# Kernel tuning notes

Measured on AMD Instinct MI355X. Metric: run time of the kernel, lower is better.

Reference implementation:

```python
import jax, jax.numpy as jnp
import numpy as np

B, L, C = 16, 4096, 32
D = 512
W = 24                  # rolling window
LAGS = [3, 5, 7]
MAXLEN = 5000
EPS = 1e-5


def setup_inputs() -> dict:
    key = jax.random.key(0)
    ks = jax.random.split(key, 8)
    return {
        "x": jax.random.normal(ks[0], (B, L, C), jnp.float32),
        "conv_w": jax.random.normal(ks[1], (D, C * (5 + len(LAGS)), 3), jnp.float32) * 0.05,
        "conv_b": jnp.zeros((D,), jnp.float32),
        "learned_pe": jax.random.normal(ks[2], (1, MAXLEN, D), jnp.float32) * (1.0 / np.sqrt(D)),
        "tape_pos": jax.random.normal(ks[3], (MAXLEN, D), jnp.float32) * 0.02,
        "tproj_w": jax.random.normal(ks[4], (D, D), jnp.float32) * 0.02,
        "tproj_b": jnp.zeros((D,), jnp.float32),
        "mixer_w": jax.random.normal(ks[5], (D, 2 * D), jnp.float32) * 0.02,
        "mixer_b": jnp.zeros((D,), jnp.float32),
        "g_c": jnp.ones((D,), jnp.float32), "b_c": jnp.zeros((D,), jnp.float32),
        "g_f": jnp.ones((D,), jnp.float32), "b_f": jnp.zeros((D,), jnp.float32),
        "g_l": jnp.ones((D,), jnp.float32), "b_l": jnp.zeros((D,), jnp.float32),
        "g_t": jnp.ones((D,), jnp.float32), "b_t": jnp.zeros((D,), jnp.float32),
        "weight_params": jnp.array([0.25, 0.25, 0.25, 0.25], jnp.float32),
    }


def _layer_norm(h, g, b):
    m = jnp.mean(h, axis=-1, keepdims=True)
    v = jnp.mean((h - m) ** 2, axis=-1, keepdims=True)
    return g * (h - m) / jnp.sqrt(v + EPS) + b


def reference(x, conv_w, conv_b, learned_pe, tape_pos, tproj_w, tproj_b,
              mixer_w, mixer_b, g_c, b_c, g_f, b_f, g_l, b_l, g_t, b_t,
              weight_params):
    Bx, Lx, Cx = x.shape
    # --- RollingFeatureExtractor: replicate-pad left, sliding mean/max/min/std
    xp = jnp.pad(x, ((0, 0), (W - 1, 0), (0, 0)), mode="edge")          # [B, L+W-1, C]
    win = jnp.stack([xp[:, i:i + Lx, :] for i in range(W)], axis=2)       # [B, L, W, C]
    w_mean = jnp.mean(win, axis=2)
    w_max = jnp.max(win, axis=2)
    w_min = jnp.min(win, axis=2)
    w_var = jnp.sum((win - w_mean[:, :, None, :]) ** 2, axis=2) / (W - 1)  # unbiased, torch.std default
    w_std = jnp.sqrt(w_var)
    x_stats = jnp.concatenate([x, w_mean, w_max, w_min, w_std], axis=-1)  # [B, L, 5C]
    # --- lag differences (replicate pad left by max lag)
    ml = max(LAGS)
    xl = jnp.pad(x, ((0, 0), (ml, 0), (0, 0)), mode="edge")
    x_lags = jnp.concatenate([x - xl[:, ml - l:ml - l + Lx, :] for l in LAGS], axis=-1)  # [B, L, 3C]
    comb = jnp.concatenate([x_stats, x_lags], axis=-1)                    # [B, L, 8C]
    # --- TokenEmbedding: Conv1d k=3, circular padding
    h = comb.transpose(0, 2, 1)                                           # [B, 8C, L]
    h = jnp.pad(h, ((0, 0), (0, 0), (1, 1)), mode="wrap")
    h = jax.lax.conv_general_dilated(h, conv_w, (1,), "VALID",
                                     dimension_numbers=("NCH", "OIH", "NCH"))
    h = h + conv_b[None, :, None]
    combined_emb = _layer_norm(h.transpose(0, 2, 1), g_c, b_c)            # [B, L, D]
    # --- fixed sinusoidal PE (constant / detached)
    pos = jnp.arange(Lx)
    div = jnp.exp(jnp.arange(0, D, 2).astype(x.dtype) * (-(np.log(10000.0) / D)))
    ang = pos[:, None].astype(x.dtype) * div[None, :]                     # [L, D/2]
    pe_fixed_tab = jnp.zeros((Lx, D), x.dtype).at[:, 0::2].set(jnp.sin(ang)).at[:, 1::2].set(jnp.cos(ang))
    pe_fixed = _layer_norm(pe_fixed_tab, g_f, b_f)[None]                  # [1, L, D]
    # --- learnable PE
    pe_learned = _layer_norm(learned_pe[:, :Lx], g_l, b_l)                # [1, L, D]
    # --- tAPE: token proj + learned pos embedding -> mixer linear
    pe = tape_pos[pos]                                                    # [L, D]
    tok = combined_emb @ tproj_w.T + tproj_b                              # [B, L, D]
    mixed = jnp.concatenate([tok, jnp.broadcast_to(pe[None], tok.shape)], axis=-1)
    pe_tape = _layer_norm(mixed @ mixer_w.T + mixer_b, g_t, b_t)          # [B, L, D]
    # --- softmax-weighted sum (dropout is identity in eval)
    w = jax.nn.softmax(weight_params)
    return (w[0] * combined_emb + w[1] * pe_fixed + w[2] * pe_learned + w[3] * pe_tape)
```

## Files before the change

kernel.cpp:

```cpp
#include <hip/hip_runtime.h>
#include <stdint.h>


typedef unsigned short u16;
using short8  = __attribute__((ext_vector_type(8))) short;
using floatx4 = __attribute__((ext_vector_type(4))) float;
typedef __attribute__((address_space(1))) const unsigned int u32_as1;
typedef __attribute__((address_space(3))) unsigned int       u32_as3;

static __device__ __forceinline__ u16 f2b(float f) {
  unsigned u = __float_as_uint(f);
  u += 0x7FFFu + ((u >> 16) & 1u);
  return (u16)(u >> 16);
}
static __device__ __forceinline__ float b2f(u16 h) {
  return __uint_as_float(((unsigned)h) << 16);
}

__global__ __launch_bounds__(256) void prep_all(
    const float* __restrict__ x,
    const float* __restrict__ conv_w, const float* __restrict__ mixer_w,
    const float* __restrict__ tproj_w, const float* __restrict__ tape_pos,
    const float* __restrict__ tproj_b, const float* __restrict__ mixer_b,
    const float* __restrict__ learned_pe,
    const float* __restrict__ gf, const float* __restrict__ bf_,
    const float* __restrict__ gl, const float* __restrict__ bl,
    u16* __restrict__ W1, u16* __restrict__ A_m1, u16* __restrict__ M2t,
    u16* __restrict__ tprojT, u16* __restrict__ tape_bf,
    float* __restrict__ bias2, u16* __restrict__ pf_tab,
    u16* __restrict__ pl_tab, u16* __restrict__ comb) {
  __shared__ float sx[87 * 32];
  const int bx = blockIdx.x;
  if (bx < 12800) {
    int i = bx * 256 + threadIdx.x;
    if (i < 393216) {
      int d = i / 768, rem = i - d * 768;
      int j = rem >> 8, c = rem & 255;
      W1[i] = f2b(conv_w[(d * 256 + c) * 3 + j]);
    } else if (i < 393216 + 262144) {
      int k = i - 393216; int p = k >> 9, r = k & 511;
      A_m1[k] = f2b(mixer_w[p * 1024 + r]);
    } else if (i < 393216 + 524288) {
      int k = i - 393216 - 262144; int p = k >> 9, r = k & 511;
      M2t[k] = f2b(mixer_w[p * 1024 + 512 + r]);
    } else if (i < 393216 + 786432) {
      int k = i - 393216 - 524288; int q = k >> 9, r = k & 511;
      tprojT[k] = f2b(tproj_w[r * 512 + q]);
    } else if (i < 393216 + 786432 + 2097152) {
      int k = i - 393216 - 786432;
      tape_bf[k] = f2b(tape_pos[k]);
    }
    return;
  }
  if (bx < 12802) {
    int p = (bx - 12800) * 256 + threadIdx.x;
    if (p < 512) {
      float s = mixer_b[p];
      for (int r = 0; r < 512; ++r) s += mixer_w[p * 1024 + r] * tproj_b[r];
      bias2[p] = s;
    }
    return;
  }
  if (bx < 13826) {
    int row = (bx - 12802) * 4 + (threadIdx.x >> 6);
    int lane = threadIdx.x & 63;
    size_t base = (size_t)row * 512 + lane * 8;
    float v[8]; float s1 = 0.f, s2 = 0.f;
    #pragma unroll
    for (int e = 0; e < 8; ++e) {
      int d = lane * 8 + e;
      int de = d & ~1;
      float div = expf((float)de * (-9.210340371976184f / 512.f));
      float ang = (float)row * div;
      v[e] = (d & 1) ? cosf(ang) : sinf(ang);
      s1 += v[e]; s2 += v[e] * v[e];
    }
    #pragma unroll
    for (int off = 32; off; off >>= 1) { s1 += __shfl_xor(s1, off); s2 += __shfl_xor(s2, off); }
    float mean = s1 * (1.f / 512.f);
    float inv = rsqrtf(fmaxf(s2 * (1.f / 512.f) - mean * mean, 0.f) + 1e-5f);
    short8 o;
    #pragma unroll
    for (int e = 0; e < 8; ++e) {
      int d = lane * 8 + e;
      o[e] = (short)f2b(gf[d] * ((v[e] - mean) * inv) + bf_[d]);
    }
    *(short8*)(pf_tab + base) = o;
    const float4* lp = (const float4*)(learned_pe + base);
    float4 a = lp[0], bq = lp[1];
    float u[8] = {a.x, a.y, a.z, a.w, bq.x, bq.y, bq.z, bq.w};
    s1 = 0.f; s2 = 0.f;
    #pragma unroll
    for (int e = 0; e < 8; ++e) { s1 += u[e]; s2 += u[e] * u[e]; }
    #pragma unroll
    for (int off = 32; off; off >>= 1) { s1 += __shfl_xor(s1, off); s2 += __shfl_xor(s2, off); }
    mean = s1 * (1.f / 512.f);
    inv = rsqrtf(fmaxf(s2 * (1.f / 512.f) - mean * mean, 0.f) + 1e-5f);
    #pragma unroll
    for (int e = 0; e < 8; ++e) {
      int d = lane * 8 + e;
      o[e] = (short)f2b(gl[d] * ((u[e] - mean) * inv) + bl[d]);
    }
    *(short8*)(pl_tab + base) = o;
    return;
  }
  const int fb = bx - 13826;
  const int b = fb >> 6, l0 = (fb & 63) * 64;
  for (int idx = threadIdx.x; idx < 87 * 32; idx += 256) {
    int r = idx >> 5, c = idx & 31;
    int ls = l0 - 23 + r; if (ls < 0) ls = 0;
    sx[idx] = x[((size_t)b * 4096 + ls) * 32 + c];
  }
  __syncthreads();
  const int c = threadIdx.x & 31, lr0 = threadIdx.x >> 5;
  for (int pass = 0; pass < 8; ++pass) {
    int lr = pass * 8 + lr0;
    int l = l0 + lr;
    float w[24];
    float s = 0.f, mx = -3.4e38f, mn = 3.4e38f;
    #pragma unroll
    for (int i = 0; i < 24; ++i) {
      float v = sx[(lr + i) * 32 + c];
      w[i] = v; s += v; mx = fmaxf(mx, v); mn = fminf(mn, v);
    }
    float mean = s * (1.f / 24.f);
    float ssd = 0.f;
    #pragma unroll
    for (int i = 0; i < 24; ++i) { float d = w[i] - mean; ssd += d * d; }
    float sd = sqrtf(fmaxf(ssd, 0.f) * (1.f / 23.f));
    float xv = w[23];
    float lag3 = xv - sx[(lr + 20) * 32 + c];
    float lag5 = xv - sx[(lr + 18) * 32 + c];
    float lag7 = xv - sx[(lr + 16) * 32 + c];
    size_t base = ((size_t)b * 4096 + l) * 256 + c;
    comb[base +   0] = f2b(xv);
    comb[base +  32] = f2b(mean);
    comb[base +  64] = f2b(mx);
    comb[base +  96] = f2b(mn);
    comb[base + 128] = f2b(sd);
    comb[base + 160] = f2b(lag3);
    comb[base + 192] = f2b(lag5);
    comb[base + 224] = f2b(lag7);
  }
}

static __device__ __forceinline__ void gemm_bt_dev(
    const u16* __restrict__ A, const u16* __restrict__ Bt,
    u16* __restrict__ outp, int K, int ldc,
    const float* __restrict__ bias, int m0, int n0,
    u16* lA, u16* lB) {
  const int tid = threadIdx.x;
  const int wave = tid >> 6, lane = tid & 63;
  const int wm = (wave & 1) * 64, wn = (wave >> 1) * 64;
  const int quad = lane >> 4, r16 = lane & 15;
  const int rowT = tid >> 3, col8 = tid & 7;

  floatx4 acc[4][4];
  #pragma unroll
  for (int i = 0; i < 4; ++i)
    #pragma unroll
    for (int j = 0; j < 4; ++j) acc[i][j] = (floatx4){0.f, 0.f, 0.f, 0.f};

  for (int kk = 0; kk < K; kk += 64) {
    __syncthreads();
    #pragma unroll
    for (int it = 0; it < 4; ++it) {
      int rr = it * 32 + rowT;
      const u16* ga = A  + (size_t)(m0 + rr) * K + kk + col8 * 8;
      const u16* gb = Bt + (size_t)(n0 + rr) * K + kk + col8 * 8;
      __builtin_amdgcn_global_load_lds((u32_as1*)ga, (u32_as3*)&lA[rr * 64 + col8 * 8], 16, 0, 0);
      __builtin_amdgcn_global_load_lds((u32_as1*)gb, (u32_as3*)&lB[rr * 64 + col8 * 8], 16, 0, 0);
    }
    __syncthreads();
    #pragma unroll
    for (int ks = 0; ks < 64; ks += 32) {
      short8 af[4], bfr[4];
      #pragma unroll
      for (int i = 0; i < 4; ++i)
        af[i] = *(const short8*)&lA[(wm + i * 16 + r16) * 64 + ks + quad * 8];
      #pragma unroll
      for (int j = 0; j < 4; ++j)
        bfr[j] = *(const short8*)&lB[(wn + j * 16 + r16) * 64 + ks + quad * 8];
      #pragma unroll
      for (int i = 0; i < 4; ++i)
        #pragma unroll
        for (int j = 0; j < 4; ++j)
          acc[i][j] = __builtin_amdgcn_mfma_f32_16x16x32_bf16(af[i], bfr[j], acc[i][j], 0, 0, 0);
    }
  }
  #pragma unroll
  for (int i = 0; i < 4; ++i) {
    #pragma unroll
    for (int rr = 0; rr < 4; ++rr) {
      int m = m0 + wm + i * 16 + quad * 4 + rr;
      #pragma unroll
      for (int j = 0; j < 4; ++j) {
        int n = n0 + wn + j * 16 + r16;
        float v = acc[i][j][rr];
        if (bias) v += bias[n];
        outp[(size_t)m * ldc + n] = f2b(v);
      }
    }
  }
}

__global__ __launch_bounds__(256) void gemm_bt_both(
    const u16* __restrict__ A_m1, const u16* __restrict__ tprojT,
    u16* __restrict__ Wf, const u16* __restrict__ tape_bf,
    const u16* __restrict__ M2t, u16* __restrict__ ctab_bf,
    const float* __restrict__ bias2) {
  __shared__ __align__(16) u16 lA[128 * 64];
  __shared__ __align__(16) u16 lB[128 * 64];
  const int bx = blockIdx.x;
  if (bx < 16) {
    gemm_bt_dev(A_m1, tprojT, Wf, 512, 512, nullptr,
                (bx & 3) * 128, (bx >> 2) * 128, lA, lB);
  } else {
    const int i = bx - 16;
    gemm_bt_dev(tape_bf, M2t, ctab_bf, 512, 512, bias2,
                (i & 31) * 128, (i >> 5) * 128, lA, lB);
  }
}


#define STAGE_A(SRCEXPR)                                                       \
  _Pragma("unroll")                                                            \
  for (int it = 0; it < 2; ++it) {                                             \
    int id = it * 256 + tid, row = id >> 3, c = id & 7;                        \
    int cg = ((c ^ (row & 7)) << 3);                                           \
    const u16* gsrc = (SRCEXPR);                                               \
    __builtin_amdgcn_global_load_lds((u32_as1*)gsrc,                           \
        (u32_as3*)(smem + id * 16), 16, 0, 0);                                 \
  }
#define STAGE_B(SRCEXPR)                                                       \
  _Pragma("unroll")                                                            \
  for (int it = 0; it < 16; ++it) {                                            \
    int id = it * 256 + tid, row = id >> 3, c = id & 7;                        \
    int cg = ((c ^ (row & 7)) << 3);                                           \
    const u16* gsrc = (SRCEXPR);                                               \
    __builtin_amdgcn_global_load_lds((u32_as1*)gsrc,                           \
        (u32_as3*)(smem + 8192 + id * 16), 16, 0, 0);                          \
  }

__global__ __launch_bounds__(256, 2) void gemm_conv_pre(
    const u16* __restrict__ comb, const u16* __restrict__ W1,
    const float* __restrict__ conv_b, const float* __restrict__ g_c,
    const float* __restrict__ b_c, const u16* __restrict__ Wf,
    const u16* __restrict__ ctab_bf, const u16* __restrict__ pf_tab,
    const u16* __restrict__ pl_tab, const float* __restrict__ g_t,
    const float* __restrict__ b_t, const float* __restrict__ wp,
    u16* __restrict__ ce, float* __restrict__ out) {
  __shared__ __align__(16) char smem[73728];
  __shared__ __align__(16) float sGB[1024];
  float* sG = sGB;
  float* sB = sGB + 512;
  u16* lA = (u16*)smem;
  u16* lB = (u16*)(smem + 8192);
  u16* lT = (u16*)smem;

  const int tid = threadIdx.x;
  if (tid < 128) {
    ((float4*)sG)[tid] = ((const float4*)g_c)[tid];
    ((float4*)sB)[tid] = ((const float4*)b_c)[tid];
  }
  const int m0 = blockIdx.x * 64;
  const int b = m0 >> 12, l0 = m0 & 4095;
  const int w = tid >> 6, lane = tid & 63;
  const int quad = lane >> 4, r16 = lane & 15;
  const int wn = w * 128;

  floatx4 acc[4][8];
  #pragma unroll
  for (int i = 0; i < 4; ++i)
    #pragma unroll
    for (int jj = 0; jj < 8; ++jj) acc[i][jj] = (floatx4){0.f, 0.f, 0.f, 0.f};

  for (int kk = 0; kk < 768; kk += 64) {
    const int jsh = kk >> 8, kc = kk & 255;
    __syncthreads();
    STAGE_A(comb + (((size_t)b * 4096 + ((l0 + row + jsh - 1 + 4096) & 4095)) << 8) + kc + cg)
    STAGE_B(W1 + (size_t)row * 768 + kk + cg)
    __syncthreads();
    #pragma unroll
    for (int ks = 0; ks < 64; ks += 32) {
      short8 af[4];
      #pragma unroll
      for (int i = 0; i < 4; ++i) {
        int row = i * 16 + r16;
        af[i] = *(const short8*)&lA[row * 64 + ((((ks >> 3) + quad) ^ (row & 7)) << 3)];
      }
      #pragma unroll
      for (int jj = 0; jj < 8; ++jj) {
        int row = wn + jj * 16 + r16;
        short8 bf = *(const short8*)&lB[row * 64 + ((((ks >> 3) + quad) ^ (row & 7)) << 3)];
        #pragma unroll
        for (int i = 0; i < 4; ++i)
          acc[i][jj] = __builtin_amdgcn_mfma_f32_16x16x32_bf16(bf, af[i], acc[i][jj], 0, 0, 0);
      }
    }
  }
  __syncthreads();
  #pragma unroll
  for (int jj = 0; jj < 8; ++jj) {
    int n = wn + jj * 16 + quad * 4;
    float4 b4 = *(const float4*)&conv_b[n];
    #pragma unroll
    for (int i = 0; i < 4; ++i) {
      ushort4 pk;
      pk.x = f2b(acc[i][jj][0] + b4.x);
      pk.y = f2b(acc[i][jj][1] + b4.y);
      pk.z = f2b(acc[i][jj][2] + b4.z);
      pk.w = f2b(acc[i][jj][3] + b4.w);
      *(ushort4*)(lT + (size_t)(i * 16 + r16) * 520 + n) = pk;
    }
  }
  __syncthreads();
  {
    const int orow = tid >> 2, part = tid & 3;
    u16* rowp = lT + (size_t)orow * 520;
    float s1 = 0.f, s2 = 0.f;
    #pragma unroll
    for (int k = 0; k < 16; ++k) {
      short8 t8 = *(const short8*)(rowp + (part + k * 4) * 8);
      #pragma unroll
      for (int e = 0; e < 8; ++e) {
        float f = b2f((u16)t8[e]); s1 += f; s2 += f * f;
      }
    }
    s1 += __shfl_xor(s1, 1); s2 += __shfl_xor(s2, 1);
    s1 += __shfl_xor(s1, 2); s2 += __shfl_xor(s2, 2);
    float mean = s1 * (1.f / 512.f);
    float inv = rsqrtf(fmaxf(s2 * (1.f / 512.f) - mean * mean, 0.f) + 1e-5f);
    size_t mrow = (size_t)(m0 + orow) * 512;
    #pragma unroll
    for (int k = 0; k < 16; ++k) {
      int c8 = part + k * 4;
      short8 t8 = *(const short8*)(rowp + c8 * 8);
      short8 o;
      #pragma unroll
      for (int e = 0; e < 8; ++e) {
        int d = c8 * 8 + e;
        o[e] = (short)f2b(sG[d] * ((b2f((u16)t8[e]) - mean) * inv) + sB[d]);
      }
      *(short8*)(ce + mrow + c8 * 8) = o;
    }
  }
  __syncthreads();
  if (tid < 128) {
    ((float4*)sG)[tid] = ((const float4*)g_t)[tid];
    ((float4*)sB)[tid] = ((const float4*)b_t)[tid];
  }

  floatx4 acc2[4][8];
  #pragma unroll
  for (int i = 0; i < 4; ++i)
    #pragma unroll
    for (int jj = 0; jj < 8; ++jj) acc2[i][jj] = (floatx4){0.f, 0.f, 0.f, 0.f};

  for (int kk = 0; kk < 512; kk += 64) {
    __syncthreads();
    STAGE_A(ce + (size_t)(m0 + row) * 512 + kk + cg)
    STAGE_B(Wf + (size_t)row * 512 + kk + cg)
    __syncthreads();
    #pragma unroll
    for (int ks = 0; ks < 64; ks += 32) {
      short8 af[4];
      #pragma unroll
      for (int i = 0; i < 4; ++i) {
        int row = i * 16 + r16;
        af[i] = *(const short8*)&lA[row * 64 + ((((ks >> 3) + quad) ^ (row & 7)) << 3)];
      }
      #pragma unroll
      for (int jj = 0; jj < 8; ++jj) {
        int row = wn + jj * 16 + r16;
        short8 bf = *(const short8*)&lB[row * 64 + ((((ks >> 3) + quad) ^ (row & 7)) << 3)];
        #pragma unroll
        for (int i = 0; i < 4; ++i)
          acc2[i][jj] = __builtin_amdgcn_mfma_f32_16x16x32_bf16(bf, af[i], acc2[i][jj], 0, 0, 0);
      }
    }
  }
  __syncthreads();
  #pragma unroll
  for (int jj = 0; jj < 8; ++jj) {
    int n = wn + jj * 16 + quad * 4;
    #pragma unroll
    for (int i = 0; i < 4; ++i) {
      ushort4 pk;
      pk.x = f2b(acc2[i][jj][0]);
      pk.y = f2b(acc2[i][jj][1]);
      pk.z = f2b(acc2[i][jj][2]);
      pk.w = f2b(acc2[i][jj][3]);
      *(ushort4*)(lT + (size_t)(i * 16 + r16) * 520 + n) = pk;
    }
  }
  __syncthreads();
  const int orow = tid >> 2, part = tid & 3;
  const int m = m0 + orow, l = l0 + orow;
  const u16* rowp = lT + (size_t)orow * 520;
  const size_t lrow = (size_t)l * 512, mrow = (size_t)m * 512;
  float s1 = 0.f, s2 = 0.f;
  #pragma unroll
  for (int k = 0; k < 16; ++k) {
    int c8 = part + k * 4;
    short8 t8 = *(const short8*)(rowp + c8 * 8);
    short8 ct = *(const short8*)(ctab_bf + lrow + c8 * 8);
    #pragma unroll
    for (int e = 0; e < 8; ++e) {
      float f = b2f((u16)t8[e]) + b2f((u16)ct[e]);
      s1 += f; s2 += f * f;
    }
  }
  s1 += __shfl_xor(s1, 1); s2 += __shfl_xor(s2, 1);
  s1 += __shfl_xor(s1, 2); s2 += __shfl_xor(s2, 2);
  float mean = s1 * (1.f / 512.f);
  float inv = rsqrtf(fmaxf(s2 * (1.f / 512.f) - mean * mean, 0.f) + 1e-5f);

  float a0 = wp[0], a1 = wp[1], a2 = wp[2], a3 = wp[3];
  float mxw = fmaxf(fmaxf(a0, a1), fmaxf(a2, a3));
  float e0 = expf(a0 - mxw), e1 = expf(a1 - mxw), e2 = expf(a2 - mxw), e3 = expf(a3 - mxw);
  float invs = 1.f / (e0 + e1 + e2 + e3);
  float w0 = e0 * invs, w1 = e1 * invs, w2 = e2 * invs, w3 = e3 * invs;

  #pragma unroll
  for (int k = 0; k < 16; ++k) {
    int c8 = part + k * 4;
    short8 t8  = *(const short8*)(rowp + c8 * 8);
    short8 ct  = *(const short8*)(ctab_bf + lrow + c8 * 8);
    short8 c8v = *(const short8*)(ce + mrow + c8 * 8);
    short8 pf  = *(const short8*)(pf_tab + lrow + c8 * 8);
    short8 pl  = *(const short8*)(pl_tab + lrow + c8 * 8);
    float o[8];
    #pragma unroll
    for (int e = 0; e < 8; ++e) {
      int d = c8 * 8 + e;
      float f = b2f((u16)t8[e]) + b2f((u16)ct[e]);
      float pt = sG[d] * ((f - mean) * inv) + sB[d];
      o[e] = w0 * b2f((u16)c8v[e]) + w1 * b2f((u16)pf[e]) + w2 * b2f((u16)pl[e]) + w3 * pt;
    }
    float4* op = (float4*)(out + mrow + c8 * 8);
    op[0] = make_float4(o[0], o[1], o[2], o[3]);
    op[1] = make_float4(o[4], o[5], o[6], o[7]);
  }
}

extern "C" void kernel_launch(void* const* d_in, const int* in_sizes, int n_in,
                              void* d_out, int out_size, void* d_ws, size_t ws_size,
                              hipStream_t stream) {
  const float* x          = (const float*)d_in[0];
  const float* conv_w     = (const float*)d_in[1];
  const float* conv_b     = (const float*)d_in[2];
  const float* learned_pe = (const float*)d_in[3];
  const float* tape_pos   = (const float*)d_in[4];
  const float* tproj_w    = (const float*)d_in[5];
  const float* tproj_b    = (const float*)d_in[6];
  const float* mixer_w    = (const float*)d_in[7];
  const float* mixer_b    = (const float*)d_in[8];
  const float* g_c        = (const float*)d_in[9];
  const float* b_c        = (const float*)d_in[10];
  const float* g_f        = (const float*)d_in[11];
  const float* b_f        = (const float*)d_in[12];
  const float* g_l        = (const float*)d_in[13];
  const float* b_l        = (const float*)d_in[14];
  const float* g_t        = (const float*)d_in[15];
  const float* b_t        = (const float*)d_in[16];
  const float* wp         = (const float*)d_in[17];

  char* ws = (char*)d_ws;
  u16*  comb    = (u16*)(ws + 0);
  u16*  ce      = (u16*)(ws + 33554432);
  char* S       = ws + 100663296;
  u16*  W1      = (u16*)(S + 0);
  u16*  A_m1    = (u16*)(S + 786432);
  u16*  M2t     = (u16*)(S + 1310720);
  u16*  tprojT  = (u16*)(S + 1835008);
  u16*  tape_bf = (u16*)(S + 2359296);
  u16*  Wf      = (u16*)(S + 6553600);
  u16*  ctab_bf = (u16*)(S + 7077888);
  float* bias2  = (float*)(S + 11272192);
  u16*  pf_tab  = (u16*)(S + 11274240);
  u16*  pl_tab  = (u16*)(S + 15468544);

  prep_all<<<14850, 256, 0, stream>>>(x, conv_w, mixer_w, tproj_w, tape_pos,
                                      tproj_b, mixer_b, learned_pe,
                                      g_f, b_f, g_l, b_l,
                                      W1, A_m1, M2t, tprojT, tape_bf,
                                      bias2, pf_tab, pl_tab, comb);
  gemm_bt_both<<<144, 256, 0, stream>>>(A_m1, tprojT, Wf, tape_bf, M2t,
                                        ctab_bf, bias2);
  gemm_conv_pre<<<1024, 256, 0, stream>>>(comb, W1, conv_b, g_c, b_c,
                                          Wf, ctab_bf, pf_tab, pl_tab,
                                          g_t, b_t, wp, ce, (float*)d_out);
}
```

Measured before the change: 356.0 us.

## Double-buffer A tiles and give each wave a private B strip in fused GEMMs

```diff
diff --git a/kernel.cpp b/kernel.cpp
--- a/kernel.cpp
+++ b/kernel.cpp
@@ -223,23 +223,23 @@
 }
 
 
-#define STAGE_A(SRCEXPR)                                                       \
+#define STAGE_A2(BUFOFF, SRCEXPR)                                              \
   _Pragma("unroll")                                                            \
   for (int it = 0; it < 2; ++it) {                                             \
     int id = it * 256 + tid, row = id >> 3, c = id & 7;                        \
     int cg = ((c ^ (row & 7)) << 3);                                           \
     const u16* gsrc = (SRCEXPR);                                               \
     __builtin_amdgcn_global_load_lds((u32_as1*)gsrc,                           \
-        (u32_as3*)(smem + id * 16), 16, 0, 0);                                 \
-  }
-#define STAGE_B(SRCEXPR)                                                       \
+        (u32_as3*)(smem + (BUFOFF) + id * 16), 16, 0, 0);                      \
+  }
+#define STRIP_B(BPTR, LDB, KK)                                                 \
   _Pragma("unroll")                                                            \
   for (int it = 0; it < 16; ++it) {                                            \
-    int id = it * 256 + tid, row = id >> 3, c = id & 7;                        \
-    int cg = ((c ^ (row & 7)) << 3);                                           \
-    const u16* gsrc = (SRCEXPR);                                               \
+    int rl = it * 8 + (lane >> 3);                                             \
+    int cgb = (((lane & 7) ^ (rl & 7)) << 3);                                  \
+    const u16* gsrc = (BPTR) + (size_t)(wn + rl) * (LDB) + (KK) + cgb;         \
     __builtin_amdgcn_global_load_lds((u32_as1*)gsrc,                           \
-        (u32_as3*)(smem + 8192 + id * 16), 16, 0, 0);                          \
+        (u32_as3*)(stripB + it * 1024 + (lane << 4)), 16, 0, 0);               \
   }
 
 __global__ __launch_bounds__(256, 2) void gemm_conv_pre(
@@ -250,24 +250,18 @@
     const u16* __restrict__ pl_tab, const float* __restrict__ g_t,
     const float* __restrict__ b_t, const float* __restrict__ wp,
     u16* __restrict__ ce, float* __restrict__ out) {
-  __shared__ __align__(16) char smem[73728];
-  __shared__ __align__(16) float sGB[1024];
-  float* sG = sGB;
-  float* sB = sGB + 512;
-  u16* lA = (u16*)smem;
-  u16* lB = (u16*)(smem + 8192);
-  u16* lT = (u16*)smem;
+  __shared__ __align__(16) char smem[81920];
+  u16*   lT = (u16*)smem;
+  float* sG = (float*)(smem + 67584);
+  float* sB = (float*)(smem + 69632);
 
   const int tid = threadIdx.x;
-  if (tid < 128) {
-    ((float4*)sG)[tid] = ((const float4*)g_c)[tid];
-    ((float4*)sB)[tid] = ((const float4*)b_c)[tid];
-  }
   const int m0 = blockIdx.x * 64;
   const int b = m0 >> 12, l0 = m0 & 4095;
   const int w = tid >> 6, lane = tid & 63;
   const int quad = lane >> 4, r16 = lane & 15;
   const int wn = w * 128;
+  char* stripB = smem + 16384 + w * 16384;
 
   floatx4 acc[4][8];
   #pragma unroll
@@ -275,28 +269,49 @@
     #pragma unroll
     for (int jj = 0; jj < 8; ++jj) acc[i][jj] = (floatx4){0.f, 0.f, 0.f, 0.f};
 
-  for (int kk = 0; kk < 768; kk += 64) {
-    const int jsh = kk >> 8, kc = kk & 255;
-    __syncthreads();
-    STAGE_A(comb + (((size_t)b * 4096 + ((l0 + row + jsh - 1 + 4096) & 4095)) << 8) + kc + cg)
-    STAGE_B(W1 + (size_t)row * 768 + kk + cg)
-    __syncthreads();
+  STAGE_A2(0, comb + (((size_t)b * 4096 + ((l0 + row - 1 + 4096) & 4095)) << 8) + cg)
+  STRIP_B(W1, 768, 0)
+
+  for (int t = 0; t < 12; ++t) {
+    const int kk = t * 64;
+    __builtin_amdgcn_sched_barrier(0);
+    __builtin_amdgcn_s_barrier();
+    __builtin_amdgcn_sched_barrier(0);
+    if (t + 1 < 12) {
+      const int kk2 = kk + 64;
+      const int jsh = kk2 >> 8, kc = kk2 & 255;
+      STAGE_A2(((t + 1) & 1) * 8192,
+          comb + (((size_t)b * 4096 + ((l0 + row + jsh - 1 + 4096) & 4095)) << 8) + kc + cg)
+      asm volatile("s_waitcnt vmcnt(2)" ::: "memory");
+    } else {
+      asm volatile("s_waitcnt vmcnt(0)" ::: "memory");
+    }
+    __builtin_amdgcn_sched_barrier(0);
+    __builtin_amdgcn_s_barrier();
+    __builtin_amdgcn_sched_barrier(0);
+    const u16* lAc = (const u16*)(smem + (t & 1) * 8192);
     #pragma unroll
     for (int ks = 0; ks < 64; ks += 32) {
       short8 af[4];
       #pragma unroll
       for (int i = 0; i < 4; ++i) {
         int row = i * 16 + r16;
-        af[i] = *(const short8*)&lA[row * 64 + ((((ks >> 3) + quad) ^ (row & 7)) << 3)];
-      }
+        af[i] = *(const short8*)&lAc[row * 64 + ((((ks >> 3) + quad) ^ (row & 7)) << 3)];
+      }
+      __builtin_amdgcn_s_setprio(1);
       #pragma unroll
       for (int jj = 0; jj < 8; ++jj) {
-        int row = wn + jj * 16 + r16;
-        short8 bf = *(const short8*)&lB[row * 64 + ((((ks >> 3) + quad) ^ (row & 7)) << 3)];
+        int rl = jj * 16 + r16;
+        short8 bf = *(const short8*)(stripB + rl * 128 + ((((ks >> 3) + quad) ^ (rl & 7)) << 4));
         #pragma unroll
         for (int i = 0; i < 4; ++i)
           acc[i][jj] = __builtin_amdgcn_mfma_f32_16x16x32_bf16(bf, af[i], acc[i][jj], 0, 0, 0);
       }
+      __builtin_amdgcn_s_setprio(0);
+    }
+    if (t + 1 < 12) {
+      const int kk2 = kk + 64;
+      STRIP_B(W1, 768, kk2)
     }
   }
   __syncthreads();
@@ -314,6 +329,10 @@
       *(ushort4*)(lT + (size_t)(i * 16 + r16) * 520 + n) = pk;
     }
   }
+  if (tid < 128) {
+    ((float4*)sG)[tid] = ((const float4*)g_c)[tid];
+    ((float4*)sB)[tid] = ((const float4*)b_c)[tid];
+  }
   __syncthreads();
   {
     const int orow = tid >> 2, part = tid & 3;
@@ -346,10 +365,6 @@
     }
   }
   __syncthreads();
-  if (tid < 128) {
-    ((float4*)sG)[tid] = ((const float4*)g_t)[tid];
-    ((float4*)sB)[tid] = ((const float4*)b_t)[tid];
-  }
 
   floatx4 acc2[4][8];
   #pragma unroll
@@ -357,27 +372,46 @@
     #pragma unroll
     for (int jj = 0; jj < 8; ++jj) acc2[i][jj] = (floatx4){0.f, 0.f, 0.f, 0.f};
 
-  for (int kk = 0; kk < 512; kk += 64) {
-    __syncthreads();
-    STAGE_A(ce + (size_t)(m0 + row) * 512 + kk + cg)
-    STAGE_B(Wf + (size_t)row * 512 + kk + cg)
-    __syncthreads();
+  STAGE_A2(0, ce + (size_t)(m0 + row) * 512 + cg)
+  STRIP_B(Wf, 512, 0)
+
+  for (int t = 0; t < 8; ++t) {
+    const int kk = t * 64;
+    __builtin_amdgcn_sched_barrier(0);
+    __builtin_amdgcn_s_barrier();
+    __builtin_amdgcn_sched_barrier(0);
+    if (t + 1 < 8) {
+      STAGE_A2(((t + 1) & 1) * 8192,
+          ce + (size_t)(m0 + row) * 512 + kk + 64 + cg)
+      asm volatile("s_waitcnt vmcnt(2)" ::: "memory");
+    } else {
+      asm volatile("s_waitcnt vmcnt(0)" ::: "memory");
+    }
+    __builtin_amdgcn_sched_barrier(0);
+    __builtin_amdgcn_s_barrier();
+    __builtin_amdgcn_sched_barrier(0);
+    const u16* lAc = (const u16*)(smem + (t & 1) * 8192);
     #pragma unroll
     for (int ks = 0; ks < 64; ks += 32) {
       short8 af[4];
       #pragma unroll
       for (int i = 0; i < 4; ++i) {
         int row = i * 16 + r16;
-        af[i] = *(const short8*)&lA[row * 64 + ((((ks >> 3) + quad) ^ (row & 7)) << 3)];
-      }
+        af[i] = *(const short8*)&lAc[row * 64 + ((((ks >> 3) + quad) ^ (row & 7)) << 3)];
+      }
+      __builtin_amdgcn_s_setprio(1);
       #pragma unroll
       for (int jj = 0; jj < 8; ++jj) {
-        int row = wn + jj * 16 + r16;
-        short8 bf = *(const short8*)&lB[row * 64 + ((((ks >> 3) + quad) ^ (row & 7)) << 3)];
+        int rl = jj * 16 + r16;
+        short8 bf = *(const short8*)(stripB + rl * 128 + ((((ks >> 3) + quad) ^ (rl & 7)) << 4));
         #pragma unroll
         for (int i = 0; i < 4; ++i)
           acc2[i][jj] = __builtin_amdgcn_mfma_f32_16x16x32_bf16(bf, af[i], acc2[i][jj], 0, 0, 0);
       }
+      __builtin_amdgcn_s_setprio(0);
+    }
+    if (t + 1 < 8) {
+      STRIP_B(Wf, 512, kk + 64)
     }
   }
   __syncthreads();
@@ -393,6 +427,10 @@
       pk.w = f2b(acc2[i][jj][3]);
       *(ushort4*)(lT + (size_t)(i * 16 + r16) * 520 + n) = pk;
     }
+  }
+  if (tid < 128) {
+    ((float4*)sG)[tid] = ((const float4*)g_t)[tid];
+    ((float4*)sB)[tid] = ((const float4*)b_t)[tid];
   }
   __syncthreads();
   const int orow = tid >> 2, part = tid & 3;
```

After: 365.2 us. 1.03x slower.

## Shrink fused conv/tAPE GEMM tile to 32 rows with 128-thread blocks

Applied to the files above, without the earlier changes.

```diff
diff --git a/kernel.cpp b/kernel.cpp
--- a/kernel.cpp
+++ b/kernel.cpp
@@ -223,26 +223,18 @@
 }
 
 
-#define STAGE_A(SRCEXPR)                                                       \
+#define STAGE_P(NLOADS, BUFOFF, SRCEXPR)                                       \
   _Pragma("unroll")                                                            \
-  for (int it = 0; it < 2; ++it) {                                             \
-    int id = it * 256 + tid, row = id >> 3, c = id & 7;                        \
-    int cg = ((c ^ (row & 7)) << 3);                                           \
+  for (int it = 0; it < NLOADS; ++it) {                                        \
+    int id = it * 128 + tid;                                                   \
+    int p = id >> 3, sres = (id & 7) ^ (p & 7);                                \
+    int r = 2 * p + (sres & 1), kc8 = (sres >> 1) << 3;                        \
     const u16* gsrc = (SRCEXPR);                                               \
     __builtin_amdgcn_global_load_lds((u32_as1*)gsrc,                           \
-        (u32_as3*)(smem + id * 16), 16, 0, 0);                                 \
-  }
-#define STAGE_B(SRCEXPR)                                                       \
-  _Pragma("unroll")                                                            \
-  for (int it = 0; it < 16; ++it) {                                            \
-    int id = it * 256 + tid, row = id >> 3, c = id & 7;                        \
-    int cg = ((c ^ (row & 7)) << 3);                                           \
-    const u16* gsrc = (SRCEXPR);                                               \
-    __builtin_amdgcn_global_load_lds((u32_as1*)gsrc,                           \
-        (u32_as3*)(smem + 8192 + id * 16), 16, 0, 0);                          \
-  }
-
-__global__ __launch_bounds__(256, 2) void gemm_conv_pre(
+        (u32_as3*)(smem + (BUFOFF) + id * 16), 16, 0, 0);                      \
+  }
+
+__global__ __launch_bounds__(128, 2) void gemm_conv_pre(
     const u16* __restrict__ comb, const u16* __restrict__ W1,
     const float* __restrict__ conv_b, const float* __restrict__ g_c,
     const float* __restrict__ b_c, const u16* __restrict__ Wf,
@@ -250,62 +242,62 @@
     const u16* __restrict__ pl_tab, const float* __restrict__ g_t,
     const float* __restrict__ b_t, const float* __restrict__ wp,
     u16* __restrict__ ce, float* __restrict__ out) {
-  __shared__ __align__(16) char smem[73728];
+  __shared__ __align__(16) char smem[34816];
   __shared__ __align__(16) float sGB[1024];
   float* sG = sGB;
   float* sB = sGB + 512;
   u16* lA = (u16*)smem;
-  u16* lB = (u16*)(smem + 8192);
+  u16* lB = (u16*)(smem + 2048);
   u16* lT = (u16*)smem;
 
   const int tid = threadIdx.x;
-  if (tid < 128) {
+  {
     ((float4*)sG)[tid] = ((const float4*)g_c)[tid];
     ((float4*)sB)[tid] = ((const float4*)b_c)[tid];
   }
-  const int m0 = blockIdx.x * 64;
+  const int m0 = blockIdx.x * 32;
   const int b = m0 >> 12, l0 = m0 & 4095;
   const int w = tid >> 6, lane = tid & 63;
   const int quad = lane >> 4, r16 = lane & 15;
-  const int wn = w * 128;
-
-  floatx4 acc[4][8];
-  #pragma unroll
-  for (int i = 0; i < 4; ++i)
-    #pragma unroll
-    for (int jj = 0; jj < 8; ++jj) acc[i][jj] = (floatx4){0.f, 0.f, 0.f, 0.f};
-
-  for (int kk = 0; kk < 768; kk += 64) {
+  const int wn = w * 256;
+  const int sl8 = ((((quad << 1) | (r16 & 1)) ^ ((r16 >> 1) & 7)) << 3);
+  const int pa0 = r16 >> 1;
+  const int pb0 = w * 128 + (r16 >> 1);
+
+  floatx4 acc[2][16];
+  #pragma unroll
+  for (int i = 0; i < 2; ++i)
+    #pragma unroll
+    for (int jj = 0; jj < 16; ++jj) acc[i][jj] = (floatx4){0.f, 0.f, 0.f, 0.f};
+
+  for (int kk = 0; kk < 768; kk += 32) {
     const int jsh = kk >> 8, kc = kk & 255;
     __syncthreads();
-    STAGE_A(comb + (((size_t)b * 4096 + ((l0 + row + jsh - 1 + 4096) & 4095)) << 8) + kc + cg)
-    STAGE_B(W1 + (size_t)row * 768 + kk + cg)
-    __syncthreads();
-    #pragma unroll
-    for (int ks = 0; ks < 64; ks += 32) {
-      short8 af[4];
-      #pragma unroll
-      for (int i = 0; i < 4; ++i) {
-        int row = i * 16 + r16;
-        af[i] = *(const short8*)&lA[row * 64 + ((((ks >> 3) + quad) ^ (row & 7)) << 3)];
-      }
-      #pragma unroll
-      for (int jj = 0; jj < 8; ++jj) {
-        int row = wn + jj * 16 + r16;
-        short8 bf = *(const short8*)&lB[row * 64 + ((((ks >> 3) + quad) ^ (row & 7)) << 3)];
-        #pragma unroll
-        for (int i = 0; i < 4; ++i)
-          acc[i][jj] = __builtin_amdgcn_mfma_f32_16x16x32_bf16(bf, af[i], acc[i][jj], 0, 0, 0);
-      }
-    }
-  }
-  __syncthreads();
-  #pragma unroll
-  for (int jj = 0; jj < 8; ++jj) {
+    STAGE_P(1, 0,
+        comb + (((size_t)b * 4096 + ((l0 + r + jsh - 1 + 4096) & 4095)) << 8) + kc + kc8)
+    STAGE_P(16, 2048, W1 + (size_t)r * 768 + kk + kc8)
+    __syncthreads();
+    short8 af[2];
+    #pragma unroll
+    for (int i = 0; i < 2; ++i)
+      af[i] = *(const short8*)&lA[(i * 8 + pa0) * 64 + sl8];
+    __builtin_amdgcn_s_setprio(1);
+    #pragma unroll
+    for (int jj = 0; jj < 16; ++jj) {
+      short8 bf = *(const short8*)&lB[(jj * 8 + pb0) * 64 + sl8];
+      #pragma unroll
+      for (int i = 0; i < 2; ++i)
+        acc[i][jj] = __builtin_amdgcn_mfma_f32_16x16x32_bf16(bf, af[i], acc[i][jj], 0, 0, 0);
+    }
+    __builtin_amdgcn_s_setprio(0);
+  }
+  __syncthreads();
+  #pragma unroll
+  for (int jj = 0; jj < 16; ++jj) {
     int n = wn + jj * 16 + quad * 4;
     float4 b4 = *(const float4*)&conv_b[n];
     #pragma unroll
-    for (int i = 0; i < 4; ++i) {
+    for (int i = 0; i < 2; ++i) {
       ushort4 pk;
       pk.x = f2b(acc[i][jj][0] + b4.x);
       pk.y = f2b(acc[i][jj][1] + b4.y);
@@ -346,46 +338,42 @@
     }
   }
   __syncthreads();
-  if (tid < 128) {
+  {
     ((float4*)sG)[tid] = ((const float4*)g_t)[tid];
     ((float4*)sB)[tid] = ((const float4*)b_t)[tid];
   }
 
-  floatx4 acc2[4][8];
-  #pragma unroll
-  for (int i = 0; i < 4; ++i)
-    #pragma unroll
-    for (int jj = 0; jj < 8; ++jj) acc2[i][jj] = (floatx4){0.f, 0.f, 0.f, 0.f};
-
-  for (int kk = 0; kk < 512; kk += 64) {
-    __syncthreads();
-    STAGE_A(ce + (size_t)(m0 + row) * 512 + kk + cg)
-    STAGE_B(Wf + (size_t)row * 512 + kk + cg)
-    __syncthreads();
-    #pragma unroll
-    for (int ks = 0; ks < 64; ks += 32) {
-      short8 af[4];
-      #pragma unroll
-      for (int i = 0; i < 4; ++i) {
-        int row = i * 16 + r16;
-        af[i] = *(const short8*)&lA[row * 64 + ((((ks >> 3) + quad) ^ (row & 7)) << 3)];
-      }
-      #pragma unroll
-      for (int jj = 0; jj < 8; ++jj) {
-        int row = wn + jj * 16 + r16;
-        short8 bf = *(const short8*)&lB[row * 64 + ((((ks >> 3) + quad) ^ (row & 7)) << 3)];
-        #pragma unroll
-        for (int i = 0; i < 4; ++i)
-          acc2[i][jj] = __builtin_amdgcn_mfma_f32_16x16x32_bf16(bf, af[i], acc2[i][jj], 0, 0, 0);
-      }
-    }
-  }
-  __syncthreads();
-  #pragma unroll
-  for (int jj = 0; jj < 8; ++jj) {
+  floatx4 acc2[2][16];
+  #pragma unroll
+  for (int i = 0; i < 2; ++i)
+    #pragma unroll
+    for (int jj = 0; jj < 16; ++jj) acc2[i][jj] = (floatx4){0.f, 0.f, 0.f, 0.f};
+
+  for (int kk = 0; kk < 512; kk += 32) {
+    __syncthreads();
+    STAGE_P(1, 0, ce + (size_t)(m0 + r) * 512 + kk + kc8)
+    STAGE_P(16, 2048, Wf + (size_t)r * 512 + kk + kc8)
+    __syncthreads();
+    short8 af[2];
+    #pragma unroll
+    for (int i = 0; i < 2; ++i)
+      af[i] = *(const short8*)&lA[(i * 8 + pa0) * 64 + sl8];
+    __builtin_amdgcn_s_setprio(1);
+    #pragma unroll
+    for (int jj = 0; jj < 16; ++jj) {
+      short8 bf = *(const short8*)&lB[(jj * 8 + pb0) * 64 + sl8];
+      #pragma unroll
+      for (int i = 0; i < 2; ++i)
+        acc2[i][jj] = __builtin_amdgcn_mfma_f32_16x16x32_bf16(bf, af[i], acc2[i][jj], 0, 0, 0);
+    }
+    __builtin_amdgcn_s_setprio(0);
+  }
+  __syncthreads();
+  #pragma unroll
+  for (int jj = 0; jj < 16; ++jj) {
     int n = wn + jj * 16 + quad * 4;
     #pragma unroll
-    for (int i = 0; i < 4; ++i) {
+    for (int i = 0; i < 2; ++i) {
       ushort4 pk;
       pk.x = f2b(acc2[i][jj][0]);
       pk.y = f2b(acc2[i][jj][1]);
@@ -488,7 +476,7 @@
                                       bias2, pf_tab, pl_tab, comb);
   gemm_bt_both<<<144, 256, 0, stream>>>(A_m1, tprojT, Wf, tape_bf, M2t,
                                         ctab_bf, bias2);
-  gemm_conv_pre<<<1024, 256, 0, stream>>>(comb, W1, conv_b, g_c, b_c,
+  gemm_conv_pre<<<2048, 128, 0, stream>>>(comb, W1, conv_b, g_c, b_c,
                                           Wf, ctab_bf, pf_tab, pl_tab,
                                           g_t, b_t, wp, ce, (float*)d_out);
 }
```

Result: slower. 493.2 us (+38.5%).
